# Kernel optimization log

Measured on AMD Instinct MI355X. Metric: run time of the kernel, lower is better.

Reference implementation:

```python
import jax, jax.numpy as jnp
import numpy as np

NUM_EMB = 512
LATENT = 128
TEXT_DIM = 512


def setup_inputs() -> dict:
    key = jax.random.key(0)
    ks = jax.random.split(key, 12)
    B, N = 64, 8192
    x = jax.random.normal(ks[0], (B, N, 3), dtype=jnp.float32)
    s = jax.random.normal(ks[1], (B, N), dtype=jnp.float32)
    e = jax.random.normal(ks[2], (B, TEXT_DIM), dtype=jnp.float32)
    # point_mlp: Linear(4,64) -> ReLU -> Linear(64,128); weights stored (in,out)
    W1 = jax.random.normal(ks[3], (4, 64), dtype=jnp.float32) * 0.5
    b1 = jnp.zeros((64,), dtype=jnp.float32)
    W2 = jax.random.normal(ks[4], (64, 128), dtype=jnp.float32) * 0.125
    b2 = jnp.zeros((128,), dtype=jnp.float32)
    # latent_mlp: Linear(128+512,256) -> ReLU -> Linear(256,128)
    W3 = jax.random.normal(ks[5], (128 + TEXT_DIM, 256), dtype=jnp.float32) * 0.04
    b3 = jnp.zeros((256,), dtype=jnp.float32)
    W4 = jax.random.normal(ks[6], (256, LATENT), dtype=jnp.float32) * 0.0625
    b4 = jnp.zeros((LATENT,), dtype=jnp.float32)
    # codebook init uniform(-1/K, 1/K) as in torch code
    codebook = jax.random.uniform(ks[7], (NUM_EMB, LATENT), dtype=jnp.float32,
                                  minval=-1.0 / NUM_EMB, maxval=1.0 / NUM_EMB)
    return {"x": x, "s": s, "e": e, "W1": W1, "b1": b1, "W2": W2, "b2": b2,
            "W3": W3, "b3": b3, "W4": W4, "b4": b4, "codebook": codebook}


def reference(x, s, e, W1, b1, W2, b2, W3, b3, W4, b4, codebook):
    # PointNet feature extraction
    point_inp = jnp.concatenate([x, s[..., None]], axis=-1)        # (B,N,4)
    h = jax.nn.relu(point_inp @ W1 + b1)                           # (B,N,64)
    point_feat = h @ W2 + b2                                       # (B,N,128)
    global_feat = jnp.max(point_feat, axis=1)                      # (B,128)
    combined = jnp.concatenate([global_feat, e], axis=-1)          # (B,640)
    z_e = jax.nn.relu(combined @ W3 + b3) @ W4 + b4                # (B,latent)
    # VQ: squared-L2 distances to codebook, argmin, gather
    dists = (jnp.sum(z_e * z_e, axis=1, keepdims=True)
             - 2.0 * (z_e @ codebook.T)
             + jnp.sum(codebook * codebook, axis=1))               # (B,K)
    indices = jnp.argmin(dists, axis=1)                            # (B,)
    z_q = codebook[indices]                                        # (B,latent)
    sg = jax.lax.stop_gradient
    codebook_loss = jnp.mean((z_q - sg(z_e)) ** 2)
    commitment_loss = jnp.mean((z_e - sg(z_q)) ** 2)
    z_q_st = z_e + sg(z_q - z_e)
    return (z_q_st, z_e, codebook_loss, commitment_loss, indices)
```

## Files before the change

kernel.cpp:

```cpp
#include <hip/hip_runtime.h>
#include <hip/hip_bf16.h>

typedef unsigned int u32;
typedef __attribute__((ext_vector_type(4))) unsigned int u32x4;
typedef __attribute__((ext_vector_type(8))) short s16x8;
typedef __attribute__((ext_vector_type(4))) float f32x4;

__device__ __forceinline__ u32 rne_hi(float a) {
    u32 u = __float_as_uint(a);
    return (u + 0x7FFFu + ((u >> 16) & 1u)) & 0xFFFF0000u;
}
__device__ __forceinline__ u32 pk_bf16(float a0, float a1) {
    __hip_bfloat162 pk2 = __float22bfloat162_rn(make_float2(a0, a1));
    u32 r;
    __builtin_memcpy(&r, &pk2, 4);
    return r;
}

__global__ __launch_bounds__(256, 4) void k1_pointfeat(
    const float* __restrict__ x, const float* __restrict__ s,
    const float* __restrict__ W1, const float* __restrict__ b1,
    const float* __restrict__ W2, float* __restrict__ ws_part)
{
    __shared__ __align__(16) u32 Hlds[2 * 2 * 64 * 32];
    const int tid   = threadIdx.x;
    const int lane  = tid & 63;
    const int point = tid & 63;
    const int kq    = __builtin_amdgcn_readfirstlane(tid >> 6);
    const int rl    = lane & 15;
    const int kg2   = lane >> 4;

    const int p0 = blockIdx.x * 512;

    s16x8 wbh[2][2], wbl[2][2];
    #pragma unroll
    for (int n = 0; n < 2; ++n)
        #pragma unroll
        for (int sl2 = 0; sl2 < 2; ++sl2)
            #pragma unroll
            for (int j = 0; j < 8; ++j) {
                float f = W2[(size_t)(kg2 * 8 + j + sl2 * 32) * 128 + kq * 32 + n * 16 + rl];
                u32 hb = rne_hi(f);
                float lo = f - __uint_as_float(hb);
                u32 lb = rne_hi(lo);
                wbh[n][sl2][j] = (short)(hb >> 16);
                wbl[n][sl2][j] = (short)(lb >> 16);
            }

    float rmax0 = -3.402823466e38f, rmax1 = -3.402823466e38f;

    const int wr0 = point * 32 + ((2 * kq)     ^ (point & 7)) * 4;
    const int wr1 = point * 32 + ((2 * kq + 1) ^ (point & 7)) * 4;

#define STAGE_COMPUTE(PX, PY, PZ, PW, VH0, VH1, VL0, VL1)                      \
    {                                                                          \
        _Pragma("unroll")                                                      \
        for (int h = 0; h < 2; ++h) {                                          \
            u32 hp[4], lp[4];                                                  \
            _Pragma("unroll")                                                  \
            for (int c = 0; c < 4; ++c) {                                      \
                const int k0 = kq * 16 + h * 8 + c * 2;                        \
                float a0 = fmaf(PX, W1[k0],                                    \
                           fmaf(PY, W1[64 + k0],                               \
                           fmaf(PZ, W1[128 + k0],                              \
                           fmaf(PW, W1[192 + k0], b1[k0]))));                  \
                float a1 = fmaf(PX, W1[k0 + 1],                                \
                           fmaf(PY, W1[65 + k0],                               \
                           fmaf(PZ, W1[129 + k0],                              \
                           fmaf(PW, W1[193 + k0], b1[k0 + 1]))));              \
                a0 = a0 > 0.f ? a0 : 0.f;                                      \
                a1 = a1 > 0.f ? a1 : 0.f;                                      \
                u32 ph = pk_bf16(a0, a1);                                      \
                float h0 = __uint_as_float(ph << 16);                          \
                float h1 = __uint_as_float(ph & 0xFFFF0000u);                  \
                u32 pl = pk_bf16(a0 - h0, a1 - h1);                            \
                hp[c] = ph; lp[c] = pl;                                        \
            }                                                                  \
            if (h == 0) { VH0 = (u32x4){hp[0],hp[1],hp[2],hp[3]};              \
                          VL0 = (u32x4){lp[0],lp[1],lp[2],lp[3]}; }            \
            else        { VH1 = (u32x4){hp[0],hp[1],hp[2],hp[3]};              \
                          VL1 = (u32x4){lp[0],lp[1],lp[2],lp[3]}; }            \
        }                                                                      \
    }
#define STAGE_WRITE(GG, VH0, VH1, VL0, VL1)                                    \
    {                                                                          \
        u32* Hw = &Hlds[((GG) & 1) * 4096];                                    \
        *(u32x4*)(Hw + wr0)        = VH0;                                      \
        *(u32x4*)(Hw + wr1)        = VH1;                                      \
        *(u32x4*)(Hw + 2048 + wr0) = VL0;                                      \
        *(u32x4*)(Hw + 2048 + wr1) = VL1;                                      \
    }

    {
        const int gp = p0 + point;
        float px = x[(size_t)gp * 3 + 0], py = x[(size_t)gp * 3 + 1];
        float pz = x[(size_t)gp * 3 + 2], pw = s[gp];
        u32x4 vh0, vh1, vl0, vl1;
        STAGE_COMPUTE(px, py, pz, pw, vh0, vh1, vl0, vl1)
        STAGE_WRITE(0, vh0, vh1, vl0, vl1)
    }
    float pxn, pyn, pzn, pwn;
    {
        const int gp = p0 + 64 + point;
        pxn = x[(size_t)gp * 3 + 0]; pyn = x[(size_t)gp * 3 + 1];
        pzn = x[(size_t)gp * 3 + 2]; pwn = s[gp];
    }

#define ARD(M, SL2) ((M) * 16 + rl) * 32 + ((((SL2) * 4 + kg2) ^ (rl & 7)) * 4)

    #pragma unroll 1
    for (int g = 0; g < 8; ++g) {
        __syncthreads();
        const u32* Hb = &Hlds[(g & 1) * 4096];

        s16x8 ah0[4], al0[4];
        #pragma unroll
        for (int m = 0; m < 4; ++m) {
            ah0[m] = *(const s16x8*)(Hb + ARD(m, 0));
            al0[m] = *(const s16x8*)(Hb + 2048 + ARD(m, 0));
        }

        u32x4 vh0, vh1, vl0, vl1;
        if (g < 7) {
            STAGE_COMPUTE(pxn, pyn, pzn, pwn, vh0, vh1, vl0, vl1)
        }

        f32x4 acc[4][2] = {};
        #pragma unroll
        for (int m = 0; m < 4; ++m)
            #pragma unroll
            for (int n = 0; n < 2; ++n)
                acc[m][n] = __builtin_amdgcn_mfma_f32_16x16x32_bf16(
                    ah0[m], wbh[n][0], acc[m][n], 0, 0, 0);
        #pragma unroll
        for (int m = 0; m < 4; ++m)
            #pragma unroll
            for (int n = 0; n < 2; ++n)
                acc[m][n] = __builtin_amdgcn_mfma_f32_16x16x32_bf16(
                    ah0[m], wbl[n][0], acc[m][n], 0, 0, 0);
        #pragma unroll
        for (int m = 0; m < 4; ++m)
            #pragma unroll
            for (int n = 0; n < 2; ++n)
                acc[m][n] = __builtin_amdgcn_mfma_f32_16x16x32_bf16(
                    al0[m], wbh[n][0], acc[m][n], 0, 0, 0);

        s16x8 ah1[4], al1[4];
        #pragma unroll
        for (int m = 0; m < 4; ++m) {
            ah1[m] = *(const s16x8*)(Hb + ARD(m, 1));
            al1[m] = *(const s16x8*)(Hb + 2048 + ARD(m, 1));
        }
        if (g < 6) {
            const int gp = p0 + (g + 2) * 64 + point;
            pxn = x[(size_t)gp * 3 + 0]; pyn = x[(size_t)gp * 3 + 1];
            pzn = x[(size_t)gp * 3 + 2]; pwn = s[gp];
        }

        #pragma unroll
        for (int m = 0; m < 4; ++m)
            #pragma unroll
            for (int n = 0; n < 2; ++n)
                acc[m][n] = __builtin_amdgcn_mfma_f32_16x16x32_bf16(
                    ah1[m], wbh[n][1], acc[m][n], 0, 0, 0);
        #pragma unroll
        for (int m = 0; m < 4; ++m)
            #pragma unroll
            for (int n = 0; n < 2; ++n)
                acc[m][n] = __builtin_amdgcn_mfma_f32_16x16x32_bf16(
                    ah1[m], wbl[n][1], acc[m][n], 0, 0, 0);
        #pragma unroll
        for (int m = 0; m < 4; ++m)
            #pragma unroll
            for (int n = 0; n < 2; ++n)
                acc[m][n] = __builtin_amdgcn_mfma_f32_16x16x32_bf16(
                    al1[m], wbh[n][1], acc[m][n], 0, 0, 0);

        if (g < 7) {
            STAGE_WRITE(g + 1, vh0, vh1, vl0, vl1)
        }

        #pragma unroll
        for (int m = 0; m < 4; ++m)
            #pragma unroll
            for (int r = 0; r < 4; ++r) {
                rmax0 = fmaxf(rmax0, acc[m][0][r]);
                rmax1 = fmaxf(rmax1, acc[m][1][r]);
            }
    }
#undef ARD
#undef STAGE_COMPUTE
#undef STAGE_WRITE

    rmax0 = fmaxf(rmax0, __shfl_xor(rmax0, 16, 64));
    rmax0 = fmaxf(rmax0, __shfl_xor(rmax0, 32, 64));
    rmax1 = fmaxf(rmax1, __shfl_xor(rmax1, 16, 64));
    rmax1 = fmaxf(rmax1, __shfl_xor(rmax1, 32, 64));
    if (lane < 16) {
        ws_part[blockIdx.x * 128 + kq * 32 + lane]      = rmax0;
        ws_part[blockIdx.x * 128 + kq * 32 + 16 + lane] = rmax1;
    }
}

__global__ __launch_bounds__(1024) void k2_head(
    const float* __restrict__ ws_part, const float* __restrict__ b2,
    const float* __restrict__ e,
    const float* __restrict__ W3, const float* __restrict__ b3,
    const float* __restrict__ W4, const float* __restrict__ b4,
    const float* __restrict__ cb, float* __restrict__ out,
    float* __restrict__ ws_loss)
{
    const int b = blockIdx.x, tid = threadIdx.x;
    __shared__ float comb[640];
    __shared__ float psum[4][256];
    __shared__ float hid[256];
    __shared__ float ze[128];
    __shared__ float red_d[512];
    __shared__ int   red_i[512];
    __shared__ float lred[128];
    __shared__ float zzs;

    if (tid < 640) {
        float v;
        if (tid < 128) {
            const float* __restrict__ pp = ws_part + (size_t)b * 16 * 128 + tid;
            float m = pp[0];
            #pragma unroll
            for (int t = 1; t < 16; ++t) m = fmaxf(m, pp[t * 128]);
            v = m + b2[tid];
        } else {
            v = e[b * 512 + (tid - 128)];
        }
        comb[tid] = v;
    }
    __syncthreads();

    {
        const int u = tid & 255, part = tid >> 8;
        const float* __restrict__ Wp = W3 + (size_t)(part * 160) * 256 + u;
        const float* __restrict__ cp = comb + part * 160;
        float a = 0.f;
        for (int i = 0; i < 160; ++i) a = fmaf(cp[i], Wp[(size_t)i * 256], a);
        psum[part][u] = a;
    }
    __syncthreads();
    if (tid < 256) {
        float hv = psum[0][tid] + psum[1][tid] + psum[2][tid] + psum[3][tid] + b3[tid];
        hid[tid] = hv > 0.f ? hv : 0.f;
    }
    __syncthreads();

    if (tid < 512) {
        const int u = tid & 127, part = tid >> 7;
        const float* __restrict__ Wp = W4 + (size_t)(part * 64) * 128 + u;
        const float* __restrict__ hp = hid + part * 64;
        float a = 0.f;
        for (int i = 0; i < 64; ++i) a = fmaf(hp[i], Wp[(size_t)i * 128], a);
        psum[part][u] = a;
    }
    __syncthreads();
    if (tid < 128) {
        float a = psum[0][tid] + psum[1][tid] + psum[2][tid] + psum[3][tid] + b4[tid];
        ze[tid] = a;
        out[8192 + b * 128 + tid] = a;
    }
    __syncthreads();

    if (tid < 64) {
        float t = ze[tid] * ze[tid] + ze[tid + 64] * ze[tid + 64];
        #pragma unroll
        for (int d = 1; d < 64; d <<= 1) t += __shfl_xor(t, d, 64);
        if (tid == 0) zzs = t;
    }
    __syncthreads();

    if (tid < 512) {
        float dot = 0.f, cc = 0.f;
        const f32x4* __restrict__ cp = (const f32x4*)(cb + (size_t)tid * 128);
        for (int k4 = 0; k4 < 32; ++k4) {
            f32x4 v = cp[k4];
            dot = fmaf(ze[k4 * 4 + 0], v.x, dot);
            cc  = fmaf(v.x, v.x, cc);
            dot = fmaf(ze[k4 * 4 + 1], v.y, dot);
            cc  = fmaf(v.y, v.y, cc);
            dot = fmaf(ze[k4 * 4 + 2], v.z, dot);
            cc  = fmaf(v.z, v.z, cc);
            dot = fmaf(ze[k4 * 4 + 3], v.w, dot);
            cc  = fmaf(v.w, v.w, cc);
        }
        red_d[tid] = zzs - 2.f * dot + cc;
        red_i[tid] = tid;
    }
    __syncthreads();

    for (int sft = 256; sft >= 1; sft >>= 1) {
        if (tid < sft) {
            float da = red_d[tid], db = red_d[tid + sft];
            int   ia = red_i[tid], ib = red_i[tid + sft];
            if (db < da || (db == da && ib < ia)) { red_d[tid] = db; red_i[tid] = ib; }
        }
        __syncthreads();
    }
    const int bc = red_i[0];

    if (tid < 128) {
        float zq  = cb[(size_t)bc * 128 + tid];
        float zev = ze[tid];
        out[b * 128 + tid] = zev + (zq - zev);
        float d = zq - zev;
        lred[tid] = d * d;
    }
    if (tid == 0) out[16386 + b] = (float)bc;
    __syncthreads();
    if (tid < 64) {
        float t = lred[tid] + lred[tid + 64];
        #pragma unroll
        for (int d = 1; d < 64; d <<= 1) t += __shfl_xor(t, d, 64);
        if (tid == 0) ws_loss[b] = t;
    }
}

__global__ void k3_loss(const float* __restrict__ ws_loss, float* __restrict__ out)
{
    const int t = threadIdx.x;
    float v = ws_loss[t];
    #pragma unroll
    for (int d = 1; d < 64; d <<= 1) v += __shfl_xor(v, d, 64);
    if (t == 0) {
        float m = v / 8192.f;
        out[16384] = m;
        out[16385] = m;
    }
}

extern "C" void kernel_launch(void* const* d_in, const int* in_sizes, int n_in,
                              void* d_out, int out_size, void* d_ws, size_t ws_size,
                              hipStream_t stream) {
    const float* x  = (const float*)d_in[0];
    const float* s  = (const float*)d_in[1];
    const float* e  = (const float*)d_in[2];
    const float* W1 = (const float*)d_in[3];
    const float* b1 = (const float*)d_in[4];
    const float* W2 = (const float*)d_in[5];
    const float* b2 = (const float*)d_in[6];
    const float* W3 = (const float*)d_in[7];
    const float* b3 = (const float*)d_in[8];
    const float* W4 = (const float*)d_in[9];
    const float* b4 = (const float*)d_in[10];
    const float* cb = (const float*)d_in[11];
    float* out = (float*)d_out;

    float* ws_part = (float*)d_ws;
    float* ws_loss = (float*)d_ws + 1024 * 128;

    k1_pointfeat<<<1024, 256, 0, stream>>>(x, s, W1, b1, W2, ws_part);
    k2_head<<<64, 1024, 0, stream>>>(ws_part, b2, e, W3, b3, W4, b4, cb, out, ws_loss);
    k3_loss<<<1, 64, 0, stream>>>(ws_loss, out);
}
```

Measured before the change: 47.98 us.

## Specialize k1 warps into producer and MFMA consumer roles

The point-feature kernel goes from 256 to 512 threads per block. Four waves now act as producers: they load points, compute the first layer with ReLU, and write the bf16 hi/lo tiles into shared memory. The other four waves hold the W2 fragments and run the MFMA accumulation and row max. This is meant to overlap the VALU-heavy first layer with the matrix work across separate waves, and to cut register pressure per wave. The cost is twice as many threads per block, half of them idle during MFMA, with the same number of barriers per stage.

```diff
diff --git a/kernel.cpp b/kernel.cpp
--- a/kernel.cpp
+++ b/kernel.cpp
@@ -17,40 +17,25 @@
     return r;
 }
 
-__global__ __launch_bounds__(256, 4) void k1_pointfeat(
+__global__ __launch_bounds__(512, 4) void k1_pointfeat(
     const float* __restrict__ x, const float* __restrict__ s,
     const float* __restrict__ W1, const float* __restrict__ b1,
     const float* __restrict__ W2, float* __restrict__ ws_part)
 {
     __shared__ __align__(16) u32 Hlds[2 * 2 * 64 * 32];
-    const int tid   = threadIdx.x;
-    const int lane  = tid & 63;
-    const int point = tid & 63;
-    const int kq    = __builtin_amdgcn_readfirstlane(tid >> 6);
+    const int tid  = threadIdx.x;
+    const int lane = tid & 63;
+    const int wid  = __builtin_amdgcn_readfirstlane(tid >> 6);
+    const int sub  = wid & 3;
+    const bool producer = wid < 4;
+    const int point = lane;
     const int rl    = lane & 15;
     const int kg2   = lane >> 4;
 
     const int p0 = blockIdx.x * 512;
 
-    s16x8 wbh[2][2], wbl[2][2];
-    #pragma unroll
-    for (int n = 0; n < 2; ++n)
-        #pragma unroll
-        for (int sl2 = 0; sl2 < 2; ++sl2)
-            #pragma unroll
-            for (int j = 0; j < 8; ++j) {
-                float f = W2[(size_t)(kg2 * 8 + j + sl2 * 32) * 128 + kq * 32 + n * 16 + rl];
-                u32 hb = rne_hi(f);
-                float lo = f - __uint_as_float(hb);
-                u32 lb = rne_hi(lo);
-                wbh[n][sl2][j] = (short)(hb >> 16);
-                wbl[n][sl2][j] = (short)(lb >> 16);
-            }
-
-    float rmax0 = -3.402823466e38f, rmax1 = -3.402823466e38f;
-
-    const int wr0 = point * 32 + ((2 * kq)     ^ (point & 7)) * 4;
-    const int wr1 = point * 32 + ((2 * kq + 1) ^ (point & 7)) * 4;
+    const int wr0 = point * 32 + ((2 * sub)     ^ (point & 7)) * 4;
+    const int wr1 = point * 32 + ((2 * sub + 1) ^ (point & 7)) * 4;
 
 #define STAGE_COMPUTE(PX, PY, PZ, PW, VH0, VH1, VL0, VL1)                      \
     {                                                                          \
@@ -59,7 +44,7 @@
             u32 hp[4], lp[4];                                                  \
             _Pragma("unroll")                                                  \
             for (int c = 0; c < 4; ++c) {                                      \
-                const int k0 = kq * 16 + h * 8 + c * 2;                        \
+                const int k0 = sub * 16 + h * 8 + c * 2;                       \
                 float a0 = fmaf(PX, W1[k0],                                    \
                            fmaf(PY, W1[64 + k0],                               \
                            fmaf(PZ, W1[128 + k0],                              \
@@ -90,115 +75,126 @@
         *(u32x4*)(Hw + 2048 + wr0) = VL0;                                      \
         *(u32x4*)(Hw + 2048 + wr1) = VL1;                                      \
     }
-
-    {
+#define ARD(M, SL2) ((M) * 16 + rl) * 32 + ((((SL2) * 4 + kg2) ^ (rl & 7)) * 4)
+
+    s16x8 wbh[2][2], wbl[2][2];
+    float rmax0 = -3.402823466e38f, rmax1 = -3.402823466e38f;
+    float pxn, pyn, pzn, pwn;
+
+    if (producer) {
         const int gp = p0 + point;
         float px = x[(size_t)gp * 3 + 0], py = x[(size_t)gp * 3 + 1];
         float pz = x[(size_t)gp * 3 + 2], pw = s[gp];
         u32x4 vh0, vh1, vl0, vl1;
         STAGE_COMPUTE(px, py, pz, pw, vh0, vh1, vl0, vl1)
         STAGE_WRITE(0, vh0, vh1, vl0, vl1)
-    }
-    float pxn, pyn, pzn, pwn;
-    {
-        const int gp = p0 + 64 + point;
-        pxn = x[(size_t)gp * 3 + 0]; pyn = x[(size_t)gp * 3 + 1];
-        pzn = x[(size_t)gp * 3 + 2]; pwn = s[gp];
-    }
-
-#define ARD(M, SL2) ((M) * 16 + rl) * 32 + ((((SL2) * 4 + kg2) ^ (rl & 7)) * 4)
+        const int gp1 = p0 + 64 + point;
+        pxn = x[(size_t)gp1 * 3 + 0]; pyn = x[(size_t)gp1 * 3 + 1];
+        pzn = x[(size_t)gp1 * 3 + 2]; pwn = s[gp1];
+    } else {
+        #pragma unroll
+        for (int n = 0; n < 2; ++n)
+            #pragma unroll
+            for (int sl2 = 0; sl2 < 2; ++sl2)
+                #pragma unroll
+                for (int j = 0; j < 8; ++j) {
+                    float f = W2[(size_t)(kg2 * 8 + j + sl2 * 32) * 128 + sub * 32 + n * 16 + rl];
+                    u32 hb = rne_hi(f);
+                    float lo = f - __uint_as_float(hb);
+                    u32 lb = rne_hi(lo);
+                    wbh[n][sl2][j] = (short)(hb >> 16);
+                    wbl[n][sl2][j] = (short)(lb >> 16);
+                }
+    }
+    __syncthreads();
 
     #pragma unroll 1
     for (int g = 0; g < 8; ++g) {
+        if (!producer) {
+            const u32* Hb = &Hlds[(g & 1) * 4096];
+            s16x8 ah0[4], al0[4];
+            #pragma unroll
+            for (int m = 0; m < 4; ++m) {
+                ah0[m] = *(const s16x8*)(Hb + ARD(m, 0));
+                al0[m] = *(const s16x8*)(Hb + 2048 + ARD(m, 0));
+            }
+            f32x4 acc[4][2] = {};
+            #pragma unroll
+            for (int m = 0; m < 4; ++m)
+                #pragma unroll
+                for (int n = 0; n < 2; ++n)
+                    acc[m][n] = __builtin_amdgcn_mfma_f32_16x16x32_bf16(
+                        ah0[m], wbh[n][0], acc[m][n], 0, 0, 0);
+            #pragma unroll
+            for (int m = 0; m < 4; ++m)
+                #pragma unroll
+                for (int n = 0; n < 2; ++n)
+                    acc[m][n] = __builtin_amdgcn_mfma_f32_16x16x32_bf16(
+                        ah0[m], wbl[n][0], acc[m][n], 0, 0, 0);
+            #pragma unroll
+            for (int m = 0; m < 4; ++m)
+                #pragma unroll
+                for (int n = 0; n < 2; ++n)
+                    acc[m][n] = __builtin_amdgcn_mfma_f32_16x16x32_bf16(
+                        al0[m], wbh[n][0], acc[m][n], 0, 0, 0);
+            s16x8 ah1[4], al1[4];
+            #pragma unroll
+            for (int m = 0; m < 4; ++m) {
+                ah1[m] = *(const s16x8*)(Hb + ARD(m, 1));
+                al1[m] = *(const s16x8*)(Hb + 2048 + ARD(m, 1));
+            }
+            #pragma unroll
+            for (int m = 0; m < 4; ++m)
+                #pragma unroll
+                for (int n = 0; n < 2; ++n)
+                    acc[m][n] = __builtin_amdgcn_mfma_f32_16x16x32_bf16(
+                        ah1[m], wbh[n][1], acc[m][n], 0, 0, 0);
+            #pragma unroll
+            for (int m = 0; m < 4; ++m)
+                #pragma unroll
+                for (int n = 0; n < 2; ++n)
+                    acc[m][n] = __builtin_amdgcn_mfma_f32_16x16x32_bf16(
+                        ah1[m], wbl[n][1], acc[m][n], 0, 0, 0);
+            #pragma unroll
+            for (int m = 0; m < 4; ++m)
+                #pragma unroll
+                for (int n = 0; n < 2; ++n)
+                    acc[m][n] = __builtin_amdgcn_mfma_f32_16x16x32_bf16(
+                        al1[m], wbh[n][1], acc[m][n], 0, 0, 0);
+            #pragma unroll
+            for (int m = 0; m < 4; ++m)
+                #pragma unroll
+                for (int r = 0; r < 4; ++r) {
+                    rmax0 = fmaxf(rmax0, acc[m][0][r]);
+                    rmax1 = fmaxf(rmax1, acc[m][1][r]);
+                }
+        } else {
+            if (g < 7) {
+                u32x4 vh0, vh1, vl0, vl1;
+                STAGE_COMPUTE(pxn, pyn, pzn, pwn, vh0, vh1, vl0, vl1)
+                STAGE_WRITE(g + 1, vh0, vh1, vl0, vl1)
+                if (g < 6) {
+                    const int gp = p0 + (g + 2) * 64 + point;
+                    pxn = x[(size_t)gp * 3 + 0]; pyn = x[(size_t)gp * 3 + 1];
+                    pzn = x[(size_t)gp * 3 + 2]; pwn = s[gp];
+                }
+            }
+        }
         __syncthreads();
-        const u32* Hb = &Hlds[(g & 1) * 4096];
-
-        s16x8 ah0[4], al0[4];
-        #pragma unroll
-        for (int m = 0; m < 4; ++m) {
-            ah0[m] = *(const s16x8*)(Hb + ARD(m, 0));
-            al0[m] = *(const s16x8*)(Hb + 2048 + ARD(m, 0));
-        }
-
-        u32x4 vh0, vh1, vl0, vl1;
-        if (g < 7) {
-            STAGE_COMPUTE(pxn, pyn, pzn, pwn, vh0, vh1, vl0, vl1)
-        }
-
-        f32x4 acc[4][2] = {};
-        #pragma unroll
-        for (int m = 0; m < 4; ++m)
-            #pragma unroll
-            for (int n = 0; n < 2; ++n)
-                acc[m][n] = __builtin_amdgcn_mfma_f32_16x16x32_bf16(
-                    ah0[m], wbh[n][0], acc[m][n], 0, 0, 0);
-        #pragma unroll
-        for (int m = 0; m < 4; ++m)
-            #pragma unroll
-            for (int n = 0; n < 2; ++n)
-                acc[m][n] = __builtin_amdgcn_mfma_f32_16x16x32_bf16(
-                    ah0[m], wbl[n][0], acc[m][n], 0, 0, 0);
-        #pragma unroll
-        for (int m = 0; m < 4; ++m)
-            #pragma unroll
-            for (int n = 0; n < 2; ++n)
-                acc[m][n] = __builtin_amdgcn_mfma_f32_16x16x32_bf16(
-                    al0[m], wbh[n][0], acc[m][n], 0, 0, 0);
-
-        s16x8 ah1[4], al1[4];
-        #pragma unroll
-        for (int m = 0; m < 4; ++m) {
-            ah1[m] = *(const s16x8*)(Hb + ARD(m, 1));
-            al1[m] = *(const s16x8*)(Hb + 2048 + ARD(m, 1));
-        }
-        if (g < 6) {
-            const int gp = p0 + (g + 2) * 64 + point;
-            pxn = x[(size_t)gp * 3 + 0]; pyn = x[(size_t)gp * 3 + 1];
-            pzn = x[(size_t)gp * 3 + 2]; pwn = s[gp];
-        }
-
-        #pragma unroll
-        for (int m = 0; m < 4; ++m)
-            #pragma unroll
-            for (int n = 0; n < 2; ++n)
-                acc[m][n] = __builtin_amdgcn_mfma_f32_16x16x32_bf16(
-                    ah1[m], wbh[n][1], acc[m][n], 0, 0, 0);
-        #pragma unroll
-        for (int m = 0; m < 4; ++m)
-            #pragma unroll
-            for (int n = 0; n < 2; ++n)
-                acc[m][n] = __builtin_amdgcn_mfma_f32_16x16x32_bf16(
-                    ah1[m], wbl[n][1], acc[m][n], 0, 0, 0);
-        #pragma unroll
-        for (int m = 0; m < 4; ++m)
-            #pragma unroll
-            for (int n = 0; n < 2; ++n)
-                acc[m][n] = __builtin_amdgcn_mfma_f32_16x16x32_bf16(
-                    al1[m], wbh[n][1], acc[m][n], 0, 0, 0);
-
-        if (g < 7) {
-            STAGE_WRITE(g + 1, vh0, vh1, vl0, vl1)
-        }
-
-        #pragma unroll
-        for (int m = 0; m < 4; ++m)
-            #pragma unroll
-            for (int r = 0; r < 4; ++r) {
-                rmax0 = fmaxf(rmax0, acc[m][0][r]);
-                rmax1 = fmaxf(rmax1, acc[m][1][r]);
-            }
     }
 #undef ARD
 #undef STAGE_COMPUTE
 #undef STAGE_WRITE
 
-    rmax0 = fmaxf(rmax0, __shfl_xor(rmax0, 16, 64));
-    rmax0 = fmaxf(rmax0, __shfl_xor(rmax0, 32, 64));
-    rmax1 = fmaxf(rmax1, __shfl_xor(rmax1, 16, 64));
-    rmax1 = fmaxf(rmax1, __shfl_xor(rmax1, 32, 64));
-    if (lane < 16) {
-        ws_part[blockIdx.x * 128 + kq * 32 + lane]      = rmax0;
-        ws_part[blockIdx.x * 128 + kq * 32 + 16 + lane] = rmax1;
+    if (!producer) {
+        rmax0 = fmaxf(rmax0, __shfl_xor(rmax0, 16, 64));
+        rmax0 = fmaxf(rmax0, __shfl_xor(rmax0, 32, 64));
+        rmax1 = fmaxf(rmax1, __shfl_xor(rmax1, 16, 64));
+        rmax1 = fmaxf(rmax1, __shfl_xor(rmax1, 32, 64));
+        if (lane < 16) {
+            ws_part[blockIdx.x * 128 + sub * 32 + lane]      = rmax0;
+            ws_part[blockIdx.x * 128 + sub * 32 + 16 + lane] = rmax1;
+        }
     }
 }
 
@@ -353,7 +349,7 @@
     float* ws_part = (float*)d_ws;
     float* ws_loss = (float*)d_ws + 1024 * 128;
 
-    k1_pointfeat<<<1024, 256, 0, stream>>>(x, s, W1, b1, W2, ws_part);
+    k1_pointfeat<<<1024, 512, 0, stream>>>(x, s, W1, b1, W2, ws_part);
     k2_head<<<64, 1024, 0, stream>>>(ws_part, b2, e, W3, b3, W4, b4, cb, out, ws_loss);
     k3_loss<<<1, 64, 0, stream>>>(ws_loss, out);
 }
```

Result: no change. 48.06 us (+0.2%).
